# Kernel optimization log

Hardware: AMD Instinct MI355X
Metric: run time of the kernel (lower is better)

Reference implementation:

```python
import jax, jax.numpy as jnp
import numpy as np

B, S, D = 4, 2048, 1024
H = 16
DH = D // H  # 64
DFF = 4096
EPS = 1e-5


def _layer_norm(x, g, b):
    mu = jnp.mean(x, axis=-1, keepdims=True)
    var = jnp.mean((x - mu) ** 2, axis=-1, keepdims=True)
    return (x - mu) * jax.lax.rsqrt(var + EPS) * g + b


def _rope(x):
    # x: [B, S, H, DH]; same rotation for every head (module reuses one RoPE).
    inv_freq = 1.0 / (10000.0 ** (jnp.arange(0, DH, 2, dtype=jnp.float32) / DH))
    pos = jnp.arange(S, dtype=jnp.float32)
    freqs = pos[:, None] * inv_freq[None, :]            # [S, DH/2]
    cos = jnp.cos(freqs)[None, :, None, :]              # [1, S, 1, DH/2]
    sin = jnp.sin(freqs)[None, :, None, :]
    x_even = x[..., 0::2]
    x_odd = x[..., 1::2]
    r_even = x_even * cos - x_odd * sin
    r_odd = x_even * sin + x_odd * cos
    return jnp.stack([r_even, r_odd], axis=-1).reshape(x.shape)


def setup_inputs() -> dict:
    key = jax.random.key(0)
    ks = jax.random.split(key, 10)
    s_d = 1.0 / np.sqrt(D)
    s_f = 1.0 / np.sqrt(DFF)
    return {
        "x": jax.random.normal(ks[0], (B, S, D), jnp.float32),
        "Wq": jax.random.uniform(ks[1], (D, D), jnp.float32, -s_d, s_d),
        "bq": jnp.zeros((D,), jnp.float32),
        "Wk": jax.random.uniform(ks[2], (D, D), jnp.float32, -s_d, s_d),
        "bk": jnp.zeros((D,), jnp.float32),
        "Wv": jax.random.uniform(ks[3], (D, D), jnp.float32, -s_d, s_d),
        "bv": jnp.zeros((D,), jnp.float32),
        "Wo": jax.random.uniform(ks[4], (D, D), jnp.float32, -s_d, s_d),
        "bo": jnp.zeros((D,), jnp.float32),
        "W1": jax.random.uniform(ks[5], (DFF, D), jnp.float32, -s_d, s_d),
        "bf1": jnp.zeros((DFF,), jnp.float32),
        "W2": jax.random.uniform(ks[6], (D, DFF), jnp.float32, -s_f, s_f),
        "bf2": jnp.zeros((D,), jnp.float32),
        "g1": jnp.ones((D,), jnp.float32),
        "be1": jnp.zeros((D,), jnp.float32),
        "g2": jnp.ones((D,), jnp.float32),
        "be2": jnp.zeros((D,), jnp.float32),
    }


def reference(x, Wq, bq, Wk, bk, Wv, bv, Wo, bo, W1, bf1, W2, bf2, g1, be1, g2, be2):
    # Pre-LN self-attention block (dropout is identity at eval)
    residual = x
    h = _layer_norm(x, g1, be1)
    q = (h @ Wq.T + bq).reshape(B, S, H, DH)
    k = (h @ Wk.T + bk).reshape(B, S, H, DH)
    v = (h @ Wv.T + bv).reshape(B, S, H, DH)
    q = _rope(q)
    k = _rope(k)
    # scores: [B, H, Sq, Sk]
    scores = jnp.einsum("bqhd,bkhd->bhqk", q, k) / np.sqrt(DH)
    causal = jnp.tril(jnp.ones((S, S), dtype=bool))
    scores = jnp.where(causal[None, None], scores, -jnp.inf)
    attn = jax.nn.softmax(scores, axis=-1)
    out = jnp.einsum("bhqk,bkhd->bqhd", attn, v).reshape(B, S, D)
    out = out @ Wo.T + bo
    x = residual + out
    # FFN block
    residual = x
    h = _layer_norm(x, g2, be2)
    ff = jax.nn.relu(h @ W1.T + bf1) @ W2.T + bf2
    return residual + ff
```

## Files before the change

### kernel.cpp

```cpp
#include <hip/hip_runtime.h>

typedef __attribute__((ext_vector_type(8))) short bh8;
typedef __attribute__((ext_vector_type(4))) short sh4;
typedef __attribute__((ext_vector_type(4))) float f4;
typedef __attribute__((ext_vector_type(16))) float f16v;
typedef __attribute__((ext_vector_type(4))) unsigned int u4;

__device__ __forceinline__ unsigned short f2bf(float x) {
  unsigned int u = __float_as_uint(x);
  u += 0x7fffu + ((u >> 16) & 1u);
  return (unsigned short)(u >> 16);
}
__device__ __forceinline__ float bf2f(short x) {
  return __uint_as_float(((unsigned int)(unsigned short)x) << 16);
}
__device__ __forceinline__ unsigned cvtpk_bf16(float lo, float hi) {
  unsigned r;
  asm("v_cvt_pk_bf16_f32 %0, %1, %2" : "=v"(r) : "v"(lo), "v"(hi));
  return r;
}
__device__ __forceinline__ void gl_lds16(const short* g, short* l) {
  __builtin_amdgcn_global_load_lds(
      (const __attribute__((address_space(1))) unsigned int*)g,
      (__attribute__((address_space(3))) unsigned int*)l, 16, 0, 0);
}

#define VM4() asm volatile("s_waitcnt vmcnt(4)" ::: "memory")
#define VM0() asm volatile("s_waitcnt vmcnt(0)" ::: "memory")

__global__ __launch_bounds__(256)
void rope_table(float* __restrict__ ct, float* __restrict__ st) {
  const int idx = blockIdx.x * 256 + threadIdx.x;
  const int s = idx >> 5, j = idx & 31;
  const float invf = expf(-0.28782313662425574f * (float)j);
  const float f = (float)s * invf;
  ct[idx] = cosf(f);
  st[idx] = sinf(f);
}

__global__ __launch_bounds__(256)
void concat_bias(const float* __restrict__ bq, const float* __restrict__ bk,
                 const float* __restrict__ bv, float* __restrict__ bqkv) {
  const int i = blockIdx.x * 256 + threadIdx.x;
  bqkv[i] = (i < 1024) ? bq[i] : ((i < 2048) ? bk[i - 1024] : bv[i - 2048]);
}

__global__ __launch_bounds__(256)
void w2bf_all(const float* __restrict__ Wq, const float* __restrict__ Wk,
              const float* __restrict__ Wv, const float* __restrict__ Wo,
              const float* __restrict__ W1, const float* __restrict__ W2,
              short* __restrict__ wqkvb, short* __restrict__ wob,
              short* __restrict__ w1b, short* __restrict__ w2b) {
  const int which = blockIdx.y;
  const float* src; short* dst; int n;
  switch (which) {
    case 0: src = Wq; dst = wqkvb;                 n = 1 << 20; break;
    case 1: src = Wk; dst = wqkvb + (1 << 20);     n = 1 << 20; break;
    case 2: src = Wv; dst = wqkvb + (2 << 20);     n = 1 << 20; break;
    case 3: src = Wo; dst = wob;                   n = 1 << 20; break;
    case 4: src = W1; dst = w1b;                   n = 1 << 22; break;
    default: src = W2; dst = w2b;                  n = 1 << 22; break;
  }
  const int i = (blockIdx.x * 256 + threadIdx.x) * 4;
  if (i >= n) return;
  f4 v = *(const f4*)(src + i);
#pragma unroll
  for (int j = 0; j < 4; ++j) dst[i + j] = (short)f2bf(v[j]);
}

__global__ __launch_bounds__(256)
void layernorm_bf(const float* __restrict__ x, const float* __restrict__ g,
                  const float* __restrict__ be, short* __restrict__ out) {
  __shared__ float sb[4];
  const int row = blockIdx.x, t = threadIdx.x;
  const float* xr = x + (size_t)row * 1024;
  f4 v = *(const f4*)(xr + t * 4);
  float s = v[0] + v[1] + v[2] + v[3];
#pragma unroll
  for (int mk = 1; mk < 64; mk <<= 1) s += __shfl_xor(s, mk, 64);
  if ((t & 63) == 0) sb[t >> 6] = s;
  __syncthreads();
  const float mean = (sb[0] + sb[1] + sb[2] + sb[3]) * (1.0f / 1024.0f);
  __syncthreads();
  f4 d;
#pragma unroll
  for (int i = 0; i < 4; ++i) d[i] = v[i] - mean;
  float s2 = d[0] * d[0] + d[1] * d[1] + d[2] * d[2] + d[3] * d[3];
#pragma unroll
  for (int mk = 1; mk < 64; mk <<= 1) s2 += __shfl_xor(s2, mk, 64);
  if ((t & 63) == 0) sb[t >> 6] = s2;
  __syncthreads();
  const float var = (sb[0] + sb[1] + sb[2] + sb[3]) * (1.0f / 1024.0f);
  const float rstd = rsqrtf(var + 1e-5f);
  const f4 gg = *(const f4*)(g + t * 4);
  const f4 bb = *(const f4*)(be + t * 4);
#pragma unroll
  for (int i = 0; i < 4; ++i)
    out[(size_t)row * 1024 + t * 4 + i] = (short)f2bf(d[i] * rstd * gg[i] + bb[i]);
}

__global__ __launch_bounds__(256)
void rope_apply(short* __restrict__ qkv, const float* __restrict__ ct,
                const float* __restrict__ st) {
  const int off = blockIdx.y ? 1024 : 0;
  const int gid = blockIdx.x * 256 + threadIdx.x;
  const int row = gid >> 7, chn = gid & 127;
  const int srow = row & 2047;
  const int col = chn * 8;
  const int j0 = (col & 63) >> 1;
  short* p = qkv + (size_t)row * 3072 + off + col;
  bh8 vv = *(const bh8*)p;
  bh8 r;
#pragma unroll
  for (int pp = 0; pp < 4; ++pp) {
    const float e = bf2f(vv[2 * pp]), od = bf2f(vv[2 * pp + 1]);
    const float c = ct[srow * 32 + j0 + pp], sn = st[srow * 32 + j0 + pp];
    r[2 * pp]     = (short)f2bf(e * c - od * sn);
    r[2 * pp + 1] = (short)f2bf(e * sn + od * c);
  }
  *(bh8*)p = r;
}

#define STG(dst, gbase, kt, half)                                              \
  {                                                                            \
    _Pragma("unroll") for (int cc = 0; cc < 2; ++cc) {                         \
      const int rr = (half) * 128 + cc * 64 + sr;                              \
      gl_lds16(gbase + (size_t)rr * K + (kt) * 64 + ssl * 8,                   \
               &dst[rr * 64 + (t & 7) * 8]);                                   \
    }                                                                          \
  }

#define PHASE(bf, q, STAGE_STMT, VMSTMT)                                       \
  {                                                                            \
    if ((q) == 0) {                                                            \
      _Pragma("unroll") for (int ni = 0; ni < 4; ++ni)                         \
      _Pragma("unroll") for (int kk = 0; kk < 2; ++kk)                         \
        bfrag[ni][kk] = *(const bh8*)(&Bs[bf][(wn * 64 + ni * 16 + (lane & 15)) * 64 + (((lane >> 4) + kk * 4) ^ (lane & 7)) * 8]); \
    }                                                                          \
    _Pragma("unroll") for (int j = 0; j < 2; ++j)                              \
    _Pragma("unroll") for (int kk = 0; kk < 2; ++kk)                           \
      af[j][kk] = *(const bh8*)(&As[bf][(wm * 128 + (2 * (q) + j) * 16 + (lane & 15)) * 64 + (((lane >> 4) + kk * 4) ^ (lane & 7)) * 8]); \
    STAGE_STMT;                                                                \
    __builtin_amdgcn_s_barrier();                                              \
    asm volatile("s_waitcnt lgkmcnt(0)" ::: "memory");                         \
    __builtin_amdgcn_sched_barrier(0);                                         \
    __builtin_amdgcn_s_setprio(1);                                             \
    _Pragma("unroll") for (int j = 0; j < 2; ++j)                              \
    _Pragma("unroll") for (int ni = 0; ni < 4; ++ni)                           \
    _Pragma("unroll") for (int kk = 0; kk < 2; ++kk)                           \
      acc[2 * (q) + j][ni] = __builtin_amdgcn_mfma_f32_16x16x32_bf16(          \
          af[j][kk], bfrag[ni][kk], acc[2 * (q) + j][ni], 0, 0, 0);            \
    __builtin_amdgcn_s_setprio(0);                                             \
    VMSTMT;                                                                    \
    __builtin_amdgcn_s_barrier();                                              \
  }

#define PH128(bf, p, STAGE_STMT, VMSTMT)                                       \
  {                                                                            \
    if ((p) == 0) {                                                            \
      _Pragma("unroll") for (int ni = 0; ni < 4; ++ni)                         \
      _Pragma("unroll") for (int kk = 0; kk < 2; ++kk)                         \
        bfrag[ni][kk] = *(const bh8*)(&Bs[bf][(wn * 64 + ni * 16 + (lane & 15)) * 64 + (((lane >> 4) + kk * 4) ^ (lane & 7)) * 8]); \
    }                                                                          \
    _Pragma("unroll") for (int j = 0; j < 2; ++j)                              \
    _Pragma("unroll") for (int kk = 0; kk < 2; ++kk)                           \
      af[j][kk] = *(const bh8*)(&As[bf][(wm * 64 + (2 * (p) + j) * 16 + (lane & 15)) * 64 + (((lane >> 4) + kk * 4) ^ (lane & 7)) * 8]); \
    STAGE_STMT;                                                                \
    __builtin_amdgcn_s_barrier();                                              \
    asm volatile("s_waitcnt lgkmcnt(0)" ::: "memory");                         \
    __builtin_amdgcn_sched_barrier(0);                                         \
    __builtin_amdgcn_s_setprio(1);                                             \
    _Pragma("unroll") for (int j = 0; j < 2; ++j)                              \
    _Pragma("unroll") for (int ni = 0; ni < 4; ++ni)                           \
    _Pragma("unroll") for (int kk = 0; kk < 2; ++kk)                           \
      acc[2 * (p) + j][ni] = __builtin_amdgcn_mfma_f32_16x16x32_bf16(          \
          af[j][kk], bfrag[ni][kk], acc[2 * (p) + j][ni], 0, 0, 0);            \
    __builtin_amdgcn_s_setprio(0);                                             \
    VMSTMT;                                                                    \
    __builtin_amdgcn_s_barrier();                                              \
  }

template <int BM, int RELU, int RES, int OBF16, int VOUT>
__global__ __launch_bounds__(512, 2)
void gemm256(const short* __restrict__ A, const short* __restrict__ Bw,
             const float* __restrict__ bias, const float* __restrict__ res,
             short* __restrict__ Vt,
             short* __restrict__ Cb, float* __restrict__ Cf,
             int M, int N, int K) {
  constexpr int MFR = BM / 128;
  constexpr int MROWS = BM / 2;
  __shared__ short As[2][BM * 64];
  __shared__ short Bs[2][256 * 64];
  const int t = threadIdx.x, lane = t & 63;
  const int w = t >> 6, wm = w >> 2, wn = w & 3;
  const int nwg = gridDim.x, cpx = nwg >> 3;
  int flat = blockIdx.x;
  flat = (flat & 7) * cpx + (flat >> 3);
  const int nbn = N >> 8;
  const int bn = flat % nbn, bm = flat / nbn;
  const short* Ab = A + (size_t)(bm * BM) * K;
  const short* Bb = Bw + (size_t)(bn * 256) * K;
  const int nkt = K >> 6;
  const int sr = t >> 3;
  const int ssl = (t & 7) ^ (sr & 7);
  f4 acc[4 * MFR][4] = {};
  bh8 bfrag[4][2], af[2][2];

  STG(Bs[0], Bb, 0, 0); STG(Bs[0], Bb, 0, 1);
  STG(As[0], Ab, 0, 0); if (BM == 256) STG(As[0], Ab, 0, 1);
  STG(Bs[1], Bb, 1, 0); STG(Bs[1], Bb, 1, 1);
  VM4();
  __builtin_amdgcn_s_barrier();

  if (BM == 256) {
    for (int i2 = 0; i2 < nkt; i2 += 2) {
      const bool nf = (i2 + 2 < nkt);
      PHASE(0, 0, STG(As[1], Ab, i2 + 1, 0), );
      PHASE(0, 1, STG(As[1], Ab, i2 + 1, 1), );
      PHASE(0, 2, if (nf) STG(Bs[0], Bb, i2 + 2, 0), );
      PHASE(0, 3, if (nf) STG(Bs[0], Bb, i2 + 2, 1),
            if (nf) { VM4(); } else { VM0(); });
      PHASE(1, 0, if (nf) STG(As[0], Ab, i2 + 2, 0), );
      PHASE(1, 1, if (nf) STG(As[0], Ab, i2 + 2, 1), );
      PHASE(1, 2, if (nf) STG(Bs[1], Bb, i2 + 3, 0), );
      PHASE(1, 3, if (nf) STG(Bs[1], Bb, i2 + 3, 1), if (nf) { VM4(); });
    }
  } else {
    for (int i2 = 0; i2 < nkt; i2 += 2) {
      const bool nf = (i2 + 2 < nkt);
      PH128(0, 0, STG(As[1], Ab, i2 + 1, 0), );
      PH128(0, 1, if (nf) { STG(Bs[0], Bb, i2 + 2, 0); STG(Bs[0], Bb, i2 + 2, 1); },
            if (nf) { VM4(); } else { VM0(); });
      PH128(1, 0, if (nf) STG(As[0], Ab, i2 + 2, 0), );
      PH128(1, 1, if (nf) { STG(Bs[1], Bb, i2 + 3, 0); STG(Bs[1], Bb, i2 + 3, 1); },
            if (nf) { VM4(); });
    }
  }

  const int rb = bm * BM + wm * MROWS + ((lane >> 4) << 2);
  const int cb = bn * 256 + wn * 64 + (lane & 15);
  if (VOUT && bn >= 8) {
#pragma unroll
    for (int mi = 0; mi < 4 * MFR; ++mi) {
#pragma unroll
      for (int ni = 0; ni < 4; ++ni) {
        const int c = cb + ni * 16;
        const float bi = bias[c];
        const int hh = (c - 2048) >> 6, dd = (c - 2048) & 63;
        const int r0 = rb + mi * 16;
        const int bb2 = r0 >> 11, ss = r0 & 2047;
        sh4 pk;
#pragma unroll
        for (int jr = 0; jr < 4; ++jr) pk[jr] = (short)f2bf(acc[mi][ni][jr] + bi);
        *(sh4*)(Vt + ((size_t)(bb2 * 16 + hh) * 64 + dd) * 2048 + ss) = pk;
      }
    }
  } else {
#pragma unroll
    for (int mi = 0; mi < 4 * MFR; ++mi) {
#pragma unroll
      for (int ni = 0; ni < 4; ++ni) {
        const int c = cb + ni * 16;
        const float bi = bias[c];
#pragma unroll
        for (int jr = 0; jr < 4; ++jr) {
          const int r = rb + mi * 16 + jr;
          float v = acc[mi][ni][jr] + bi;
          if (RES) v += res[(size_t)r * N + c];
          if (RELU) v = fmaxf(v, 0.f);
          if (OBF16) Cb[(size_t)r * N + c] = (short)f2bf(v);
          else       Cf[(size_t)r * N + c] = v;
        }
      }
    }
  }
}

__global__ __launch_bounds__(512, 2)
void flash_attn(const short* __restrict__ qkv, const short* __restrict__ vt,
                short* __restrict__ o) {
  __shared__ short lds[2 * 2 * 64 * 72];
  const int t = threadIdx.x, lane = t & 63, w = t >> 6;
  const int l31 = lane & 31, l5 = lane >> 5;
  const int id = blockIdx.x;
  const int xcd = id & 7, y = id >> 3;
  const int bh = xcd * 8 + (y >> 2);
  const int pr = y & 3;
  const int b = bh >> 4, hh = bh & 15;
  const int r8 = t >> 3, c8 = (t & 7) * 8;
  const float NEG_INF = -__builtin_inff();

  const short* kbase = qkv + (size_t)b * 2048 * 3072 + 1024 + hh * 64;
  const short* vbase = vt + ((size_t)bh * 64 + r8) * 2048;

  for (int pass = 0; pass < 2; ++pass) {
    const int qt = pass ? pr : 7 - pr;
    const int wq0 = qt * 256 + w * 32;
    const int nt = 4 * qt + 4;

    bh8 qf[4];
    {
      const short* qrow = qkv + ((size_t)b * 2048 + wq0 + l31) * 3072 + hh * 64 + l5 * 8;
#pragma unroll
      for (int dk = 0; dk < 4; ++dk) qf[dk] = *(const bh8*)(qrow + dk * 16);
    }
    f16v o0 = {}, o1 = {};
    float mr = NEG_INF, lsum = 0.f;

    __syncthreads();
    {
      bh8 rk = *(const bh8*)(kbase + (size_t)r8 * 3072 + c8);
      bh8 rv = *(const bh8*)(vbase + c8);
      *(bh8*)(&lds[r8 * 72 + c8]) = rk;
      *(bh8*)(&lds[4608 + r8 * 72 + c8]) = rv;
    }

    for (int kt = 0; kt < nt; ++kt) {
      __syncthreads();
      const int cur = kt & 1, nxt = cur ^ 1;
      bh8 rk, rv;
      const bool more = (kt + 1 < nt);
      if (more) {
        rk = *(const bh8*)(kbase + (size_t)((kt + 1) * 64 + r8) * 3072 + c8);
        rv = *(const bh8*)(vbase + (kt + 1) * 64 + c8);
      }
      const int kvb = kt * 64;
      if (kvb <= wq0 + 31) {
        const short* Kl = &lds[cur * 9216];
        const short* Vl = &lds[cur * 9216 + 4608];
        f16v s0 = {}, s1 = {};
#pragma unroll
        for (int dk = 0; dk < 4; ++dk) {
          bh8 ka0 = *(const bh8*)(&Kl[l31 * 72 + dk * 16 + l5 * 8]);
          bh8 ka1 = *(const bh8*)(&Kl[(32 + l31) * 72 + dk * 16 + l5 * 8]);
          s0 = __builtin_amdgcn_mfma_f32_32x32x16_bf16(ka0, qf[dk], s0, 0, 0, 0);
          s1 = __builtin_amdgcn_mfma_f32_32x32x16_bf16(ka1, qf[dk], s1, 0, 0, 0);
        }
        if (kvb + 63 > wq0) {
          const int qq = wq0 + l31;
          const int kvo = kvb + l5 * 4;
#pragma unroll
          for (int r = 0; r < 16; ++r) {
            const int kv0 = kvo + (r & 3) + 8 * (r >> 2);
            if (kv0 > qq) s0[r] = NEG_INF;
            if (kv0 + 32 > qq) s1[r] = NEG_INF;
          }
        }
        float mx = s0[0];
#pragma unroll
        for (int r = 1; r < 16; ++r) mx = fmaxf(mx, s0[r]);
#pragma unroll
        for (int r = 0; r < 16; ++r) mx = fmaxf(mx, s1[r]);
        mx = fmaxf(mx, __shfl_xor(mx, 32, 64));
        const bool keep = __all(mx <= mr + 8.0f);
        float mn, al;
        if (keep) { mn = mr; al = 1.0f; }
        else {
          mn = fmaxf(mr, mx);
          al = __expf((mr - mn) * 0.125f);
          mr = mn;
        }
        float rsA = 0.f, rsB = 0.f;
#pragma unroll
        for (int r = 0; r < 16; ++r) {
          const float p0 = __expf((s0[r] - mn) * 0.125f);
          const float p1 = __expf((s1[r] - mn) * 0.125f);
          s0[r] = p0; s1[r] = p1;
          rsA += p0; rsB += p1;
        }
        float rs = rsA + rsB;
        rs += __shfl_xor(rs, 32, 64);
        if (keep) {
          lsum += rs;
        } else {
          lsum = lsum * al + rs;
#pragma unroll
          for (int r = 0; r < 16; ++r) { o0[r] *= al; o1[r] *= al; }
        }
        float pp[32];
#pragma unroll
        for (int r = 0; r < 16; ++r) { pp[r] = s0[r]; pp[16 + r] = s1[r]; }
        const bool lo32 = (l5 == 0);
#pragma unroll
        for (int ks = 0; ks < 4; ++ks) {
          const int base = (ks >> 1) * 16 + (ks & 1) * 8;
          const unsigned e0 = cvtpk_bf16(pp[base + 0], pp[base + 1]);
          const unsigned e1 = cvtpk_bf16(pp[base + 2], pp[base + 3]);
          const unsigned q0 = cvtpk_bf16(pp[base + 4], pp[base + 5]);
          const unsigned q1 = cvtpk_bf16(pp[base + 6], pp[base + 7]);
          const unsigned sel0 = lo32 ? q0 : e0;
          const unsigned sel1 = lo32 ? q1 : e1;
          const unsigned rx0 = (unsigned)__shfl_xor((int)sel0, 32, 64);
          const unsigned rx1 = (unsigned)__shfl_xor((int)sel1, 32, 64);
          u4 frag;
          frag[0] = lo32 ? e0 : rx0;
          frag[1] = lo32 ? e1 : rx1;
          frag[2] = lo32 ? rx0 : q0;
          frag[3] = lo32 ? rx1 : q1;
          const bh8 pb = *(const bh8*)&frag;
          bh8 va0 = *(const bh8*)(&Vl[l31 * 72 + ks * 16 + l5 * 8]);
          bh8 va1 = *(const bh8*)(&Vl[(32 + l31) * 72 + ks * 16 + l5 * 8]);
          o0 = __builtin_amdgcn_mfma_f32_32x32x16_bf16(va0, pb, o0, 0, 0, 0);
          o1 = __builtin_amdgcn_mfma_f32_32x32x16_bf16(va1, pb, o1, 0, 0, 0);
        }
      }
      if (more) {
        *(bh8*)(&lds[nxt * 9216 + r8 * 72 + c8]) = rk;
        *(bh8*)(&lds[nxt * 9216 + 4608 + r8 * 72 + c8]) = rv;
      }
    }

    const float inv = 1.0f / lsum;
    __syncthreads();
    short* Ot = lds;
#pragma unroll
    for (int r = 0; r < 16; ++r) {
      const int d = (r & 3) + 8 * (r >> 2) + 4 * l5;
      Ot[(w * 32 + l31) * 72 + d]      = (short)f2bf(o0[r] * inv);
      Ot[(w * 32 + l31) * 72 + 32 + d] = (short)f2bf(o1[r] * inv);
    }
    __syncthreads();
    const int qrow = t >> 1, half = t & 1;
    short* orow = o + ((size_t)b * 2048 + qt * 256 + qrow) * 1024 + hh * 64 + half * 32;
#pragma unroll
    for (int i = 0; i < 4; ++i)
      *(bh8*)(orow + i * 8) = *(const bh8*)(&Ot[qrow * 72 + half * 32 + i * 8]);
  }
}

extern "C" void kernel_launch(void* const* d_in, const int* in_sizes, int n_in,
                              void* d_out, int out_size, void* d_ws, size_t ws_size,
                              hipStream_t stream) {
  const float* x   = (const float*)d_in[0];
  const float* Wq  = (const float*)d_in[1];
  const float* bq  = (const float*)d_in[2];
  const float* Wk  = (const float*)d_in[3];
  const float* bk  = (const float*)d_in[4];
  const float* Wv  = (const float*)d_in[5];
  const float* bv  = (const float*)d_in[6];
  const float* Wo  = (const float*)d_in[7];
  const float* bo  = (const float*)d_in[8];
  const float* W1  = (const float*)d_in[9];
  const float* bf1 = (const float*)d_in[10];
  const float* W2  = (const float*)d_in[11];
  const float* bf2 = (const float*)d_in[12];
  const float* g1  = (const float*)d_in[13];
  const float* be1 = (const float*)d_in[14];
  const float* g2  = (const float*)d_in[15];
  const float* be2 = (const float*)d_in[16];
  float* out = (float*)d_out;

  char* ws = (char*)d_ws;
  const size_t MB = 1u << 20;
  short* h_ob  = (short*)ws;
  short* qkv   = (short*)(ws + 16 * MB);
  short* f1    = (short*)(ws + 16 * MB);
  short* vtb   = (short*)(ws + 64 * MB);
  short* wqkvb = (short*)(ws + 80 * MB);
  short* wob   = (short*)(ws + 86 * MB);
  short* w1b   = (short*)(ws + 88 * MB);
  short* w2b   = (short*)(ws + 96 * MB);
  float* ct    = (float*)(ws + 104 * MB);
  float* st    = ct + 65536;
  float* bqkv  = st + 65536;
  float* x2    = out;

  rope_table<<<256, 256, 0, stream>>>(ct, st);
  concat_bias<<<12, 256, 0, stream>>>(bq, bk, bv, bqkv);
  w2bf_all<<<dim3(4096, 6), 256, 0, stream>>>(Wq, Wk, Wv, Wo, W1, W2,
                                              wqkvb, wob, w1b, w2b);

  layernorm_bf<<<8192, 256, 0, stream>>>(x, g1, be1, h_ob);

  gemm256<128, 0, 0, 1, 1><<<768, 512, 0, stream>>>(h_ob, wqkvb, bqkv, nullptr, vtb, qkv, nullptr, 8192, 3072, 1024);

  rope_apply<<<dim3(4096, 2), 256, 0, stream>>>(qkv, ct, st);

  flash_attn<<<256, 512, 0, stream>>>(qkv, vtb, h_ob);

  gemm256<128, 0, 1, 0, 0><<<256, 512, 0, stream>>>(h_ob, wob, bo, x, nullptr, nullptr, x2, 8192, 1024, 1024);

  layernorm_bf<<<8192, 256, 0, stream>>>(x2, g2, be2, h_ob);

  gemm256<256, 1, 0, 1, 0><<<512, 512, 0, stream>>>(h_ob, w1b, bf1, nullptr, nullptr, f1, nullptr, 8192, 4096, 1024);

  gemm256<128, 0, 1, 0, 0><<<256, 512, 0, stream>>>(f1, w2b, bf2, x2, nullptr, nullptr, out, 8192, 1024, 4096);
}
```

Measured before the change: 378.6 us.

## Split flash-attention passes into separate blocks and add 128x128 GEMM for N=1024

Flash attention now launches 512 blocks, each handling one query tile instead of looping over a paired short and long tile, so twice as many workgroups are in flight. The two N=1024 projections (output and FFN down) switch to a new 128x128-tile GEMM with four blocks per CU, which doubles the grid from 256 to 512 workgroups on a 256-CU part. The residual add moves entirely into the new kernel and gemm256 loses its RES path. The cost is lower per-block data reuse, more A/B traffic from L2, and less balanced attention work per block, since the causal tiles no longer pair a short with a long one.

After: 361.3 us. 4.6% less time.

```diff
diff --git a/kernel.cpp b/kernel.cpp
--- a/kernel.cpp
+++ b/kernel.cpp
@@ -26,6 +26,7 @@
 }
 
 #define VM4() asm volatile("s_waitcnt vmcnt(4)" ::: "memory")
+#define VM2() asm volatile("s_waitcnt vmcnt(2)" ::: "memory")
 #define VM0() asm volatile("s_waitcnt vmcnt(0)" ::: "memory")
 
 __global__ __launch_bounds__(256)
@@ -139,7 +140,7 @@
     }                                                                          \
     _Pragma("unroll") for (int j = 0; j < 2; ++j)                              \
     _Pragma("unroll") for (int kk = 0; kk < 2; ++kk)                           \
-      af[j][kk] = *(const bh8*)(&As[bf][(wm * 128 + (2 * (q) + j) * 16 + (lane & 15)) * 64 + (((lane >> 4) + kk * 4) ^ (lane & 7)) * 8]); \
+      af[j][kk] = *(const bh8*)(&As[bf][(wm * MROWS + (2 * (q) + j) * 16 + (lane & 15)) * 64 + (((lane >> 4) + kk * 4) ^ (lane & 7)) * 8]); \
     STAGE_STMT;                                                                \
     __builtin_amdgcn_s_barrier();                                              \
     asm volatile("s_waitcnt lgkmcnt(0)" ::: "memory");                         \
@@ -155,39 +156,13 @@
     __builtin_amdgcn_s_barrier();                                              \
   }
 
-#define PH128(bf, p, STAGE_STMT, VMSTMT)                                       \
-  {                                                                            \
-    if ((p) == 0) {                                                            \
-      _Pragma("unroll") for (int ni = 0; ni < 4; ++ni)                         \
-      _Pragma("unroll") for (int kk = 0; kk < 2; ++kk)                         \
-        bfrag[ni][kk] = *(const bh8*)(&Bs[bf][(wn * 64 + ni * 16 + (lane & 15)) * 64 + (((lane >> 4) + kk * 4) ^ (lane & 7)) * 8]); \
-    }                                                                          \
-    _Pragma("unroll") for (int j = 0; j < 2; ++j)                              \
-    _Pragma("unroll") for (int kk = 0; kk < 2; ++kk)                           \
-      af[j][kk] = *(const bh8*)(&As[bf][(wm * 64 + (2 * (p) + j) * 16 + (lane & 15)) * 64 + (((lane >> 4) + kk * 4) ^ (lane & 7)) * 8]); \
-    STAGE_STMT;                                                                \
-    __builtin_amdgcn_s_barrier();                                              \
-    asm volatile("s_waitcnt lgkmcnt(0)" ::: "memory");                         \
-    __builtin_amdgcn_sched_barrier(0);                                         \
-    __builtin_amdgcn_s_setprio(1);                                             \
-    _Pragma("unroll") for (int j = 0; j < 2; ++j)                              \
-    _Pragma("unroll") for (int ni = 0; ni < 4; ++ni)                           \
-    _Pragma("unroll") for (int kk = 0; kk < 2; ++kk)                           \
-      acc[2 * (p) + j][ni] = __builtin_amdgcn_mfma_f32_16x16x32_bf16(          \
-          af[j][kk], bfrag[ni][kk], acc[2 * (p) + j][ni], 0, 0, 0);            \
-    __builtin_amdgcn_s_setprio(0);                                             \
-    VMSTMT;                                                                    \
-    __builtin_amdgcn_s_barrier();                                              \
-  }
-
-template <int BM, int RELU, int RES, int OBF16, int VOUT>
+template <int BM, int RELU, int OBF16, int VOUT>
 __global__ __launch_bounds__(512, 2)
 void gemm256(const short* __restrict__ A, const short* __restrict__ Bw,
-             const float* __restrict__ bias, const float* __restrict__ res,
+             const float* __restrict__ bias,
              short* __restrict__ Vt,
              short* __restrict__ Cb, float* __restrict__ Cf,
              int M, int N, int K) {
-  constexpr int MFR = BM / 128;
   constexpr int MROWS = BM / 2;
   __shared__ short As[2][BM * 64];
   __shared__ short Bs[2][256 * 64];
@@ -203,7 +178,7 @@
   const int nkt = K >> 6;
   const int sr = t >> 3;
   const int ssl = (t & 7) ^ (sr & 7);
-  f4 acc[4 * MFR][4] = {};
+  f4 acc[BM / 32][4] = {};
   bh8 bfrag[4][2], af[2][2];
 
   STG(Bs[0], Bb, 0, 0); STG(Bs[0], Bb, 0, 1);
@@ -228,11 +203,11 @@
   } else {
     for (int i2 = 0; i2 < nkt; i2 += 2) {
       const bool nf = (i2 + 2 < nkt);
-      PH128(0, 0, STG(As[1], Ab, i2 + 1, 0), );
-      PH128(0, 1, if (nf) { STG(Bs[0], Bb, i2 + 2, 0); STG(Bs[0], Bb, i2 + 2, 1); },
+      PHASE(0, 0, STG(As[1], Ab, i2 + 1, 0), );
+      PHASE(0, 1, if (nf) { STG(Bs[0], Bb, i2 + 2, 0); STG(Bs[0], Bb, i2 + 2, 1); },
             if (nf) { VM4(); } else { VM0(); });
-      PH128(1, 0, if (nf) STG(As[0], Ab, i2 + 2, 0), );
-      PH128(1, 1, if (nf) { STG(Bs[1], Bb, i2 + 3, 0); STG(Bs[1], Bb, i2 + 3, 1); },
+      PHASE(1, 0, if (nf) STG(As[0], Ab, i2 + 2, 0), );
+      PHASE(1, 1, if (nf) { STG(Bs[1], Bb, i2 + 3, 0); STG(Bs[1], Bb, i2 + 3, 1); },
             if (nf) { VM4(); });
     }
   }
@@ -241,7 +216,7 @@
   const int cb = bn * 256 + wn * 64 + (lane & 15);
   if (VOUT && bn >= 8) {
 #pragma unroll
-    for (int mi = 0; mi < 4 * MFR; ++mi) {
+    for (int mi = 0; mi < BM / 32; ++mi) {
 #pragma unroll
       for (int ni = 0; ni < 4; ++ni) {
         const int c = cb + ni * 16;
@@ -257,7 +232,7 @@
     }
   } else {
 #pragma unroll
-    for (int mi = 0; mi < 4 * MFR; ++mi) {
+    for (int mi = 0; mi < BM / 32; ++mi) {
 #pragma unroll
       for (int ni = 0; ni < 4; ++ni) {
         const int c = cb + ni * 16;
@@ -266,7 +241,6 @@
         for (int jr = 0; jr < 4; ++jr) {
           const int r = rb + mi * 16 + jr;
           float v = acc[mi][ni][jr] + bi;
-          if (RES) v += res[(size_t)r * N + c];
           if (RELU) v = fmaxf(v, 0.f);
           if (OBF16) Cb[(size_t)r * N + c] = (short)f2bf(v);
           else       Cf[(size_t)r * N + c] = v;
@@ -276,156 +250,236 @@
   }
 }
 
-__global__ __launch_bounds__(512, 2)
+#define PH64(bf, q, STAGE_STMT, VMSTMT)                                        \
+  {                                                                            \
+    if ((q) == 0) {                                                            \
+      _Pragma("unroll") for (int ni = 0; ni < 2; ++ni)                         \
+      _Pragma("unroll") for (int kk = 0; kk < 2; ++kk)                         \
+        bfrag[ni][kk] = *(const bh8*)(&Bs[bf][(wn * 32 + ni * 16 + (lane & 15)) * 64 + (((lane >> 4) + kk * 4) ^ (lane & 7)) * 8]); \
+    }                                                                          \
+    _Pragma("unroll") for (int j = 0; j < 2; ++j)                              \
+    _Pragma("unroll") for (int kk = 0; kk < 2; ++kk)                           \
+      af[j][kk] = *(const bh8*)(&As[bf][(wm * 64 + (2 * (q) + j) * 16 + (lane & 15)) * 64 + (((lane >> 4) + kk * 4) ^ (lane & 7)) * 8]); \
+    STAGE_STMT;                                                                \
+    __builtin_amdgcn_s_barrier();                                              \
+    asm volatile("s_waitcnt lgkmcnt(0)" ::: "memory");                         \
+    __builtin_amdgcn_sched_barrier(0);                                         \
+    __builtin_amdgcn_s_setprio(1);                                             \
+    _Pragma("unroll") for (int j = 0; j < 2; ++j)                              \
+    _Pragma("unroll") for (int ni = 0; ni < 2; ++ni)                           \
+    _Pragma("unroll") for (int kk = 0; kk < 2; ++kk)                           \
+      acc[2 * (q) + j][ni] = __builtin_amdgcn_mfma_f32_16x16x32_bf16(          \
+          af[j][kk], bfrag[ni][kk], acc[2 * (q) + j][ni], 0, 0, 0);            \
+    __builtin_amdgcn_s_setprio(0);                                             \
+    VMSTMT;                                                                    \
+    __builtin_amdgcn_s_barrier();                                              \
+  }
+
+template <int RELU, int RES, int OBF16>
+__global__ __launch_bounds__(512, 4)
+void gemm_bn128(const short* __restrict__ A, const short* __restrict__ Bw,
+                const float* __restrict__ bias, const float* __restrict__ res,
+                short* __restrict__ Cb, float* __restrict__ Cf,
+                int M, int N, int K) {
+  __shared__ short As[2][128 * 64];
+  __shared__ short Bs[2][128 * 64];
+  const int t = threadIdx.x, lane = t & 63;
+  const int w = t >> 6, wm = w >> 2, wn = w & 3;
+  const int nwg = gridDim.x, cpx = nwg >> 3;
+  int flat = blockIdx.x;
+  flat = (flat & 7) * cpx + (flat >> 3);
+  const int nbn = N >> 7;
+  const int bn = flat % nbn, bm = flat / nbn;
+  const short* Ab = A + (size_t)(bm * 128) * K;
+  const short* Bb = Bw + (size_t)(bn * 128) * K;
+  const int nkt = K >> 6;
+  const int sr = t >> 3;
+  const int ssl = (t & 7) ^ (sr & 7);
+  f4 acc[4][2] = {};
+  bh8 bfrag[2][2], af[2][2];
+
+  STG(Bs[0], Bb, 0, 0); STG(As[0], Ab, 0, 0);
+  STG(Bs[1], Bb, 1, 0);
+  VM2();
+  __builtin_amdgcn_s_barrier();
+
+  for (int i2 = 0; i2 < nkt; i2 += 2) {
+    const bool nf = (i2 + 2 < nkt);
+    PH64(0, 0, STG(As[1], Ab, i2 + 1, 0), );
+    PH64(0, 1, if (nf) STG(Bs[0], Bb, i2 + 2, 0),
+         if (nf) { VM2(); } else { VM0(); });
+    PH64(1, 0, if (nf) STG(As[0], Ab, i2 + 2, 0), );
+    PH64(1, 1, if (nf) STG(Bs[1], Bb, i2 + 3, 0), if (nf) { VM2(); });
+  }
+
+  const int rb = bm * 128 + wm * 64 + ((lane >> 4) << 2);
+  const int cb = bn * 128 + wn * 32 + (lane & 15);
+#pragma unroll
+  for (int mi = 0; mi < 4; ++mi) {
+#pragma unroll
+    for (int ni = 0; ni < 2; ++ni) {
+      const int c = cb + ni * 16;
+      const float bi = bias[c];
+#pragma unroll
+      for (int jr = 0; jr < 4; ++jr) {
+        const int r = rb + mi * 16 + jr;
+        float v = acc[mi][ni][jr] + bi;
+        if (RES) v += res[(size_t)r * N + c];
+        if (RELU) v = fmaxf(v, 0.f);
+        if (OBF16) Cb[(size_t)r * N + c] = (short)f2bf(v);
+        else       Cf[(size_t)r * N + c] = v;
+      }
+    }
+  }
+}
+
+__global__ __launch_bounds__(512, 4)
 void flash_attn(const short* __restrict__ qkv, const short* __restrict__ vt,
                 short* __restrict__ o) {
   __shared__ short lds[2 * 2 * 64 * 72];
   const int t = threadIdx.x, lane = t & 63, w = t >> 6;
   const int l31 = lane & 31, l5 = lane >> 5;
   const int id = blockIdx.x;
-  const int xcd = id & 7, y = id >> 3;
+  const int half = id >> 8, j = id & 255;
+  const int xcd = j & 7, y = j >> 3;
   const int bh = xcd * 8 + (y >> 2);
   const int pr = y & 3;
+  const int qt = half ? pr : 7 - pr;
   const int b = bh >> 4, hh = bh & 15;
   const int r8 = t >> 3, c8 = (t & 7) * 8;
   const float NEG_INF = -__builtin_inff();
 
   const short* kbase = qkv + (size_t)b * 2048 * 3072 + 1024 + hh * 64;
   const short* vbase = vt + ((size_t)bh * 64 + r8) * 2048;
-
-  for (int pass = 0; pass < 2; ++pass) {
-    const int qt = pass ? pr : 7 - pr;
-    const int wq0 = qt * 256 + w * 32;
-    const int nt = 4 * qt + 4;
-
-    bh8 qf[4];
-    {
-      const short* qrow = qkv + ((size_t)b * 2048 + wq0 + l31) * 3072 + hh * 64 + l5 * 8;
-#pragma unroll
-      for (int dk = 0; dk < 4; ++dk) qf[dk] = *(const bh8*)(qrow + dk * 16);
-    }
-    f16v o0 = {}, o1 = {};
-    float mr = NEG_INF, lsum = 0.f;
-
+  const int wq0 = qt * 256 + w * 32;
+  const int nt = 4 * qt + 4;
+
+  bh8 qf[4];
+  {
+    const short* qrow = qkv + ((size_t)b * 2048 + wq0 + l31) * 3072 + hh * 64 + l5 * 8;
+#pragma unroll
+    for (int dk = 0; dk < 4; ++dk) qf[dk] = *(const bh8*)(qrow + dk * 16);
+  }
+  f16v o0 = {}, o1 = {};
+  float mr = NEG_INF, lsum = 0.f;
+
+  {
+    bh8 rk = *(const bh8*)(kbase + (size_t)r8 * 3072 + c8);
+    bh8 rv = *(const bh8*)(vbase + c8);
+    *(bh8*)(&lds[r8 * 72 + c8]) = rk;
+    *(bh8*)(&lds[4608 + r8 * 72 + c8]) = rv;
+  }
+
+  for (int kt = 0; kt < nt; ++kt) {
     __syncthreads();
-    {
-      bh8 rk = *(const bh8*)(kbase + (size_t)r8 * 3072 + c8);
-      bh8 rv = *(const bh8*)(vbase + c8);
-      *(bh8*)(&lds[r8 * 72 + c8]) = rk;
-      *(bh8*)(&lds[4608 + r8 * 72 + c8]) = rv;
-    }
-
-    for (int kt = 0; kt < nt; ++kt) {
-      __syncthreads();
-      const int cur = kt & 1, nxt = cur ^ 1;
-      bh8 rk, rv;
-      const bool more = (kt + 1 < nt);
-      if (more) {
-        rk = *(const bh8*)(kbase + (size_t)((kt + 1) * 64 + r8) * 3072 + c8);
-        rv = *(const bh8*)(vbase + (kt + 1) * 64 + c8);
-      }
-      const int kvb = kt * 64;
-      if (kvb <= wq0 + 31) {
-        const short* Kl = &lds[cur * 9216];
-        const short* Vl = &lds[cur * 9216 + 4608];
-        f16v s0 = {}, s1 = {};
-#pragma unroll
-        for (int dk = 0; dk < 4; ++dk) {
-          bh8 ka0 = *(const bh8*)(&Kl[l31 * 72 + dk * 16 + l5 * 8]);
-          bh8 ka1 = *(const bh8*)(&Kl[(32 + l31) * 72 + dk * 16 + l5 * 8]);
-          s0 = __builtin_amdgcn_mfma_f32_32x32x16_bf16(ka0, qf[dk], s0, 0, 0, 0);
-          s1 = __builtin_amdgcn_mfma_f32_32x32x16_bf16(ka1, qf[dk], s1, 0, 0, 0);
+    const int cur = kt & 1, nxt = cur ^ 1;
+    bh8 rk, rv;
+    const bool more = (kt + 1 < nt);
+    if (more) {
+      rk = *(const bh8*)(kbase + (size_t)((kt + 1) * 64 + r8) * 3072 + c8);
+      rv = *(const bh8*)(vbase + (kt + 1) * 64 + c8);
+    }
+    const int kvb = kt * 64;
+    if (kvb <= wq0 + 31) {
+      const short* Kl = &lds[cur * 9216];
+      const short* Vl = &lds[cur * 9216 + 4608];
+      f16v s0 = {}, s1 = {};
+#pragma unroll
+      for (int dk = 0; dk < 4; ++dk) {
+        bh8 ka0 = *(const bh8*)(&Kl[l31 * 72 + dk * 16 + l5 * 8]);
+        bh8 ka1 = *(const bh8*)(&Kl[(32 + l31) * 72 + dk * 16 + l5 * 8]);
+        s0 = __builtin_amdgcn_mfma_f32_32x32x16_bf16(ka0, qf[dk], s0, 0, 0, 0);
+        s1 = __builtin_amdgcn_mfma_f32_32x32x16_bf16(ka1, qf[dk], s1, 0, 0, 0);
+      }
+      if (kvb + 63 > wq0) {
+        const int qq = wq0 + l31;
+        const int kvo = kvb + l5 * 4;
+#pragma unroll
+        for (int r = 0; r < 16; ++r) {
+          const int kv0 = kvo + (r & 3) + 8 * (r >> 2);
+          if (kv0 > qq) s0[r] = NEG_INF;
+          if (kv0 + 32 > qq) s1[r] = NEG_INF;
         }
-        if (kvb + 63 > wq0) {
-          const int qq = wq0 + l31;
-          const int kvo = kvb + l5 * 4;
-#pragma unroll
-          for (int r = 0; r < 16; ++r) {
-            const int kv0 = kvo + (r & 3) + 8 * (r >> 2);
-            if (kv0 > qq) s0[r] = NEG_INF;
-            if (kv0 + 32 > qq) s1[r] = NEG_INF;
-          }
-        }
-        float mx = s0[0];
-#pragma unroll
-        for (int r = 1; r < 16; ++r) mx = fmaxf(mx, s0[r]);
-#pragma unroll
-        for (int r = 0; r < 16; ++r) mx = fmaxf(mx, s1[r]);
-        mx = fmaxf(mx, __shfl_xor(mx, 32, 64));
-        const bool keep = __all(mx <= mr + 8.0f);
-        float mn, al;
-        if (keep) { mn = mr; al = 1.0f; }
-        else {
-          mn = fmaxf(mr, mx);
-          al = __expf((mr - mn) * 0.125f);
-          mr = mn;
-        }
-        float rsA = 0.f, rsB = 0.f;
-#pragma unroll
-        for (int r = 0; r < 16; ++r) {
-          const float p0 = __expf((s0[r] - mn) * 0.125f);
-          const float p1 = __expf((s1[r] - mn) * 0.125f);
-          s0[r] = p0; s1[r] = p1;
-          rsA += p0; rsB += p1;
-        }
-        float rs = rsA + rsB;
-        rs += __shfl_xor(rs, 32, 64);
-        if (keep) {
-          lsum += rs;
-        } else {
-          lsum = lsum * al + rs;
-#pragma unroll
-          for (int r = 0; r < 16; ++r) { o0[r] *= al; o1[r] *= al; }
-        }
-        float pp[32];
-#pragma unroll
-        for (int r = 0; r < 16; ++r) { pp[r] = s0[r]; pp[16 + r] = s1[r]; }
-        const bool lo32 = (l5 == 0);
-#pragma unroll
-        for (int ks = 0; ks < 4; ++ks) {
-          const int base = (ks >> 1) * 16 + (ks & 1) * 8;
-          const unsigned e0 = cvtpk_bf16(pp[base + 0], pp[base + 1]);
-          const unsigned e1 = cvtpk_bf16(pp[base + 2], pp[base + 3]);
-          const unsigned q0 = cvtpk_bf16(pp[base + 4], pp[base + 5]);
-          const unsigned q1 = cvtpk_bf16(pp[base + 6], pp[base + 7]);
-          const unsigned sel0 = lo32 ? q0 : e0;
-          const unsigned sel1 = lo32 ? q1 : e1;
-          const unsigned rx0 = (unsigned)__shfl_xor((int)sel0, 32, 64);
-          const unsigned rx1 = (unsigned)__shfl_xor((int)sel1, 32, 64);
-          u4 frag;
-          frag[0] = lo32 ? e0 : rx0;
-          frag[1] = lo32 ? e1 : rx1;
-          frag[2] = lo32 ? rx0 : q0;
-          frag[3] = lo32 ? rx1 : q1;
-          const bh8 pb = *(const bh8*)&frag;
-          bh8 va0 = *(const bh8*)(&Vl[l31 * 72 + ks * 16 + l5 * 8]);
-          bh8 va1 = *(const bh8*)(&Vl[(32 + l31) * 72 + ks * 16 + l5 * 8]);
-          o0 = __builtin_amdgcn_mfma_f32_32x32x16_bf16(va0, pb, o0, 0, 0, 0);
-          o1 = __builtin_amdgcn_mfma_f32_32x32x16_bf16(va1, pb, o1, 0, 0, 0);
-        }
-      }
-      if (more) {
-        *(bh8*)(&lds[nxt * 9216 + r8 * 72 + c8]) = rk;
-        *(bh8*)(&lds[nxt * 9216 + 4608 + r8 * 72 + c8]) = rv;
-      }
-    }
-
-    const float inv = 1.0f / lsum;
-    __syncthreads();
-    short* Ot = lds;
-#pragma unroll
-    for (int r = 0; r < 16; ++r) {
-      const int d = (r & 3) + 8 * (r >> 2) + 4 * l5;
-      Ot[(w * 32 + l31) * 72 + d]      = (short)f2bf(o0[r] * inv);
-      Ot[(w * 32 + l31) * 72 + 32 + d] = (short)f2bf(o1[r] * inv);
-    }
-    __syncthreads();
-    const int qrow = t >> 1, half = t & 1;
-    short* orow = o + ((size_t)b * 2048 + qt * 256 + qrow) * 1024 + hh * 64 + half * 32;
-#pragma unroll
-    for (int i = 0; i < 4; ++i)
-      *(bh8*)(orow + i * 8) = *(const bh8*)(&Ot[qrow * 72 + half * 32 + i * 8]);
-  }
+      }
+      float mx = s0[0];
+#pragma unroll
+      for (int r = 1; r < 16; ++r) mx = fmaxf(mx, s0[r]);
+#pragma unroll
+      for (int r = 0; r < 16; ++r) mx = fmaxf(mx, s1[r]);
+      mx = fmaxf(mx, __shfl_xor(mx, 32, 64));
+      const bool keep = __all(mx <= mr + 8.0f);
+      float mn, al;
+      if (keep) { mn = mr; al = 1.0f; }
+      else {
+        mn = fmaxf(mr, mx);
+        al = __expf((mr - mn) * 0.125f);
+        mr = mn;
+      }
+      float rsA = 0.f, rsB = 0.f;
+#pragma unroll
+      for (int r = 0; r < 16; ++r) {
+        const float p0 = __expf((s0[r] - mn) * 0.125f);
+        const float p1 = __expf((s1[r] - mn) * 0.125f);
+        s0[r] = p0; s1[r] = p1;
+        rsA += p0; rsB += p1;
+      }
+      float rs = rsA + rsB;
+      rs += __shfl_xor(rs, 32, 64);
+      if (keep) {
+        lsum += rs;
+      } else {
+        lsum = lsum * al + rs;
+#pragma unroll
+        for (int r = 0; r < 16; ++r) { o0[r] *= al; o1[r] *= al; }
+      }
+      float pp[32];
+#pragma unroll
+      for (int r = 0; r < 16; ++r) { pp[r] = s0[r]; pp[16 + r] = s1[r]; }
+      const bool lo32 = (l5 == 0);
+#pragma unroll
+      for (int ks = 0; ks < 4; ++ks) {
+        const int base = (ks >> 1) * 16 + (ks & 1) * 8;
+        const unsigned e0 = cvtpk_bf16(pp[base + 0], pp[base + 1]);
+        const unsigned e1 = cvtpk_bf16(pp[base + 2], pp[base + 3]);
+        const unsigned q0 = cvtpk_bf16(pp[base + 4], pp[base + 5]);
+        const unsigned q1 = cvtpk_bf16(pp[base + 6], pp[base + 7]);
+        const unsigned sel0 = lo32 ? q0 : e0;
+        const unsigned sel1 = lo32 ? q1 : e1;
+        const unsigned rx0 = (unsigned)__shfl_xor((int)sel0, 32, 64);
+        const unsigned rx1 = (unsigned)__shfl_xor((int)sel1, 32, 64);
+        u4 frag;
+        frag[0] = lo32 ? e0 : rx0;
+        frag[1] = lo32 ? e1 : rx1;
+        frag[2] = lo32 ? rx0 : q0;
+        frag[3] = lo32 ? rx1 : q1;
+        const bh8 pb = *(const bh8*)&frag;
+        bh8 va0 = *(const bh8*)(&Vl[l31 * 72 + ks * 16 + l5 * 8]);
+        bh8 va1 = *(const bh8*)(&Vl[(32 + l31) * 72 + ks * 16 + l5 * 8]);
+        o0 = __builtin_amdgcn_mfma_f32_32x32x16_bf16(va0, pb, o0, 0, 0, 0);
+        o1 = __builtin_amdgcn_mfma_f32_32x32x16_bf16(va1, pb, o1, 0, 0, 0);
+      }
+    }
+    if (more) {
+      *(bh8*)(&lds[nxt * 9216 + r8 * 72 + c8]) = rk;
+      *(bh8*)(&lds[nxt * 9216 + 4608 + r8 * 72 + c8]) = rv;
+    }
+  }
+
+  const float inv = 1.0f / lsum;
+  __syncthreads();
+  short* Ot = lds;
+#pragma unroll
+  for (int r = 0; r < 16; ++r) {
+    const int d = (r & 3) + 8 * (r >> 2) + 4 * l5;
+    Ot[(w * 32 + l31) * 72 + d]      = (short)f2bf(o0[r] * inv);
+    Ot[(w * 32 + l31) * 72 + 32 + d] = (short)f2bf(o1[r] * inv);
+  }
+  __syncthreads();
+  const int qrow = t >> 1, hf = t & 1;
+  short* orow = o + ((size_t)b * 2048 + qt * 256 + qrow) * 1024 + hh * 64 + hf * 32;
+#pragma unroll
+  for (int i = 0; i < 4; ++i)
+    *(bh8*)(orow + i * 8) = *(const bh8*)(&Ot[qrow * 72 + hf * 32 + i * 8]);
 }
 
 extern "C" void kernel_launch(void* const* d_in, const int* in_sizes, int n_in,
@@ -472,17 +526,17 @@
 
   layernorm_bf<<<8192, 256, 0, stream>>>(x, g1, be1, h_ob);
 
-  gemm256<128, 0, 0, 1, 1><<<768, 512, 0, stream>>>(h_ob, wqkvb, bqkv, nullptr, vtb, qkv, nullptr, 8192, 3072, 1024);
+  gemm256<128, 0, 1, 1><<<768, 512, 0, stream>>>(h_ob, wqkvb, bqkv, vtb, qkv, nullptr, 8192, 3072, 1024);
 
   rope_apply<<<dim3(4096, 2), 256, 0, stream>>>(qkv, ct, st);
 
-  flash_attn<<<256, 512, 0, stream>>>(qkv, vtb, h_ob);
-
-  gemm256<128, 0, 1, 0, 0><<<256, 512, 0, stream>>>(h_ob, wob, bo, x, nullptr, nullptr, x2, 8192, 1024, 1024);
+  flash_attn<<<512, 512, 0, stream>>>(qkv, vtb, h_ob);
+
+  gemm_bn128<0, 1, 0><<<512, 512, 0, stream>>>(h_ob, wob, bo, x, nullptr, x2, 8192, 1024, 1024);
 
   layernorm_bf<<<8192, 256, 0, stream>>>(x2, g2, be2, h_ob);
 
-  gemm256<256, 1, 0, 1, 0><<<512, 512, 0, stream>>>(h_ob, w1b, bf1, nullptr, nullptr, f1, nullptr, 8192, 4096, 1024);
-
-  gemm256<128, 0, 1, 0, 0><<<256, 512, 0, stream>>>(f1, w2b, bf2, x2, nullptr, nullptr, out, 8192, 1024, 4096);
-}
+  gemm256<256, 1, 1, 0><<<512, 512, 0, stream>>>(h_ob, w1b, bf1, nullptr, f1, nullptr, 8192, 4096, 1024);
+
+  gemm_bn128<0, 1, 0><<<512, 512, 0, stream>>>(f1, w2b, bf2, x2, nullptr, out, 8192, 1024, 4096);
+}
```
